# Kernel optimization log

Hardware: AMD Instinct MI355X
Metric: run time of the kernel (lower is better)

Reference implementation:

```python
import math
import jax, jax.numpy as jnp
import numpy as np

B, T, D = 32, 2048, 512
FACTOR = 2
TOP_K = int(FACTOR * math.log(T))  # = 15, static (T is static under jit)


def setup_inputs() -> dict:
    key = jax.random.key(0)
    ks = jax.random.split(key, 11)
    s = 1.0 / math.sqrt(D)
    return {
        "query": jax.random.normal(ks[0], (B, T, D), jnp.float32),
        "key_in": jax.random.normal(ks[1], (B, T, D), jnp.float32),
        "value": jax.random.normal(ks[2], (B, T, D), jnp.float32),
        "Wq": jax.random.normal(ks[3], (D, D), jnp.float32) * s,
        "bq": jnp.zeros((D,), jnp.float32),
        "Wk": jax.random.normal(ks[4], (D, D), jnp.float32) * s,
        "bk": jnp.zeros((D,), jnp.float32),
        "Wv": jax.random.normal(ks[5], (D, D), jnp.float32) * s,
        "bv": jnp.zeros((D,), jnp.float32),
        "Wo": jax.random.normal(ks[6], (D, D), jnp.float32) * s,
        "bo": jnp.zeros((D,), jnp.float32),
    }


def reference(query, key_in, value, Wq, bq, Wk, bk, Wv, bv, Wo, bo):
    # Linear projections (query/key/value lengths are equal here, so no trimming)
    q = query @ Wq + bq      # [B, T, D]
    k = key_in @ Wk + bk     # [B, T, D]
    v = value @ Wv + bv      # [B, T, D]

    # FFT cross-correlation along the time axis
    qf = jnp.fft.rfft(q, axis=1)
    kf = jnp.fft.rfft(k, axis=1)
    attn_weights = jnp.fft.irfft(qf * jnp.conj(kf), n=T, axis=1)  # [B, T, D]

    # Top-k delay selection on the feature-mean autocorrelation
    autocorr_mean = attn_weights.mean(axis=-1)           # [B, T]
    _, topk_delays = jax.lax.top_k(autocorr_mean, TOP_K)  # [B, K] int32

    # Sum of circularly-rolled values over the top-k delays.
    # tf.roll(v, s, 0): out[t] = v[(t - s) mod T]; accumulate via scan over K
    def body(acc, d):  # d: [B] delays for this k
        rolled = jax.vmap(lambda vb, db: jnp.roll(vb, db, axis=0))(v, d)
        return acc + rolled, None

    rolled_sum, _ = jax.lax.scan(body, jnp.zeros_like(v), topk_delays.T)  # [B, T, D]

    # Softmax over the feature axis (independent of k in the original loop)
    soft_attn = jax.nn.softmax(attn_weights, axis=-1)    # [B, T, D]
    attn_output = rolled_sum * soft_attn                 # [B, T, D]

    return attn_output @ Wo + bo
```

## Files before the change

kernel.cpp:

```cpp
#include <hip/hip_runtime.h>

#define NFFT 2048
#define LDK 40
#define FFT_PAD(p) ((p) + ((p) >> 5))

typedef __attribute__((ext_vector_type(8))) short bf16x8;
typedef __attribute__((ext_vector_type(4))) float f32x4;

__device__ __forceinline__ unsigned short f2bf_rne(float x) {
  unsigned u = __float_as_uint(x);
  return (unsigned short)((u + 0x7fffu + ((u >> 16) & 1u)) >> 16);
}
__device__ __forceinline__ float bf2f(unsigned short h) {
  return __uint_as_float(((unsigned)h) << 16);
}

__global__ __launch_bounds__(256) void wsplit_kernel(
    const float* __restrict__ W0, const float* __restrict__ W1,
    const float* __restrict__ W2, const float* __restrict__ W3,
    unsigned short* __restrict__ out) {
  __shared__ float tile[32][33];
  const float* W = (blockIdx.z == 0) ? W0
                   : (blockIdx.z == 1) ? W1
                   : (blockIdx.z == 2) ? W2 : W3;
  unsigned short* hi = out + (size_t)blockIdx.z * 524288;
  unsigned short* lo = hi + 262144;
  const int k0 = blockIdx.x * 32, n0 = blockIdx.y * 32;
  const int c = threadIdx.x & 31, r = threadIdx.x >> 5;
#pragma unroll
  for (int p = 0; p < 4; p++)
    tile[r + 8 * p][c] = W[(size_t)(k0 + r + 8 * p) * 512 + n0 + c];
  __syncthreads();
#pragma unroll
  for (int p = 0; p < 4; p++) {
    int nn = r + 8 * p;
    float x = tile[c][nn];
    unsigned u = __float_as_uint(x);
    unsigned short h = (unsigned short)(u >> 16);
    float hf = __uint_as_float(u & 0xffff0000u);
    unsigned short l = f2bf_rne(x - hf);
    hi[(size_t)(n0 + nn) * 512 + k0 + c] = h;
    lo[(size_t)(n0 + nn) * 512 + k0 + c] = l;
  }
}

__global__ __launch_bounds__(256) void proj_gemm_split(
    const float* __restrict__ X, const unsigned short* __restrict__ WThi,
    const unsigned short* __restrict__ WTlo, const float* __restrict__ bias,
    float* __restrict__ YT) {
  __shared__ __align__(16) unsigned short Wh[128 * LDK];
  __shared__ __align__(16) unsigned short Wl[128 * LDK];
  __shared__ __align__(16) unsigned short Xh[128 * LDK];
  __shared__ __align__(16) unsigned short Xl[128 * LDK];
  const int tid = threadIdx.x;
  const int n0 = blockIdx.x * 128;
  const int b = blockIdx.y >> 4;
  const int t0 = (blockIdx.y & 15) * 128;
  const int w = tid >> 6, l = tid & 63;
  const int wn = (w & 1) * 64;
  const int wt = (w >> 1) * 64;
  const int fr = l & 15;
  const int fk = (l >> 4) * 8;

  f32x4 acc[4][4];
#pragma unroll
  for (int i = 0; i < 4; i++)
#pragma unroll
    for (int j = 0; j < 4; j++) acc[i][j] = (f32x4)0.f;

  const int srow = tid >> 1, scol = (tid & 1) * 16;
  const float* Xg = X + ((size_t)(b * 2048 + t0 + srow)) * 512 + scol;
  const unsigned short* Whg = WThi + ((size_t)(n0 + srow)) * 512 + scol;
  const unsigned short* Wlg = WTlo + ((size_t)(n0 + srow)) * 512 + scol;
  unsigned short* XhL = &Xh[srow * LDK + scol];
  unsigned short* XlL = &Xl[srow * LDK + scol];
  unsigned short* WhL = &Wh[srow * LDK + scol];
  unsigned short* WlL = &Wl[srow * LDK + scol];

  for (int k0 = 0; k0 < 512; k0 += 32) {
    float xv[16];
    *(float4*)&xv[0] = *(const float4*)&Xg[k0];
    *(float4*)&xv[4] = *(const float4*)&Xg[k0 + 4];
    *(float4*)&xv[8] = *(const float4*)&Xg[k0 + 8];
    *(float4*)&xv[12] = *(const float4*)&Xg[k0 + 12];
    uint4 wh0 = *(const uint4*)&Whg[k0];
    uint4 wh1 = *(const uint4*)&Whg[k0 + 8];
    uint4 wl0 = *(const uint4*)&Wlg[k0];
    uint4 wl1 = *(const uint4*)&Wlg[k0 + 8];
    union { unsigned short us[16]; uint4 q[2]; } hb, lb;
#pragma unroll
    for (int i = 0; i < 16; i++) {
      unsigned u = __float_as_uint(xv[i]);
      hb.us[i] = (unsigned short)(u >> 16);
      float hf = __uint_as_float(u & 0xffff0000u);
      lb.us[i] = f2bf_rne(xv[i] - hf);
    }
    __syncthreads();
    *(uint4*)&XhL[0] = hb.q[0];
    *(uint4*)&XhL[8] = hb.q[1];
    *(uint4*)&XlL[0] = lb.q[0];
    *(uint4*)&XlL[8] = lb.q[1];
    *(uint4*)&WhL[0] = wh0;
    *(uint4*)&WhL[8] = wh1;
    *(uint4*)&WlL[0] = wl0;
    *(uint4*)&WlL[8] = wl1;
    __syncthreads();
    bf16x8 ah[4], al[4], bh[4], bl[4];
#pragma unroll
    for (int i = 0; i < 4; i++) {
      ah[i] = *(const bf16x8*)&Wh[(wn + 16 * i + fr) * LDK + fk];
      al[i] = *(const bf16x8*)&Wl[(wn + 16 * i + fr) * LDK + fk];
      bh[i] = *(const bf16x8*)&Xh[(wt + 16 * i + fr) * LDK + fk];
      bl[i] = *(const bf16x8*)&Xl[(wt + 16 * i + fr) * LDK + fk];
    }
#pragma unroll
    for (int i = 0; i < 4; i++)
#pragma unroll
      for (int j = 0; j < 4; j++) {
        acc[i][j] = __builtin_amdgcn_mfma_f32_16x16x32_bf16(ah[i], bh[j],
                                                            acc[i][j], 0, 0, 0);
        acc[i][j] = __builtin_amdgcn_mfma_f32_16x16x32_bf16(al[i], bh[j],
                                                            acc[i][j], 0, 0, 0);
        acc[i][j] = __builtin_amdgcn_mfma_f32_16x16x32_bf16(ah[i], bl[j],
                                                            acc[i][j], 0, 0, 0);
      }
  }
  const size_t obase = (size_t)b * 512 * 2048;
#pragma unroll
  for (int i = 0; i < 4; i++) {
#pragma unroll
    for (int r = 0; r < 4; r++) {
      int n = n0 + wn + 16 * i + (l >> 4) * 4 + r;
      float bsc = bias[n];
      size_t row = obase + (size_t)n * 2048 + t0 + wt + (l & 15);
#pragma unroll
      for (int j = 0; j < 4; j++) YT[row + 16 * j] = acc[i][j][r] + bsc;
    }
  }
}

__global__ __launch_bounds__(256) void gemm_bf16_vproj(
    const float* __restrict__ X, const unsigned short* __restrict__ WThi,
    const float* __restrict__ bias, unsigned short* __restrict__ Vbf) {
  __shared__ __align__(16) unsigned short Ws[128 * LDK];
  __shared__ __align__(16) unsigned short Xs[128 * LDK];
  const int tid = threadIdx.x;
  const int n0 = blockIdx.x * 128;
  const int b = blockIdx.y >> 4;
  const int t0 = (blockIdx.y & 15) * 128;
  const int w = tid >> 6, l = tid & 63;
  const int wr = (w & 1) * 64;
  const int wc = (w >> 1) * 64;
  const int fr = l & 15, fk = (l >> 4) * 8;

  f32x4 acc[4][4];
#pragma unroll
  for (int i = 0; i < 4; i++)
#pragma unroll
    for (int j = 0; j < 4; j++) acc[i][j] = (f32x4)0.f;

  const int srow = tid >> 1, scol = (tid & 1) * 16;
  const float* Xg = X + ((size_t)(b * 2048 + t0 + srow)) * 512 + scol;
  const unsigned short* Wg = WThi + ((size_t)(n0 + srow)) * 512 + scol;
  unsigned short* XsL = &Xs[srow * LDK + scol];
  unsigned short* WsL = &Ws[srow * LDK + scol];

  for (int k0 = 0; k0 < 512; k0 += 32) {
    float xv[16];
    *(float4*)&xv[0] = *(const float4*)&Xg[k0];
    *(float4*)&xv[4] = *(const float4*)&Xg[k0 + 4];
    *(float4*)&xv[8] = *(const float4*)&Xg[k0 + 8];
    *(float4*)&xv[12] = *(const float4*)&Xg[k0 + 12];
    uint4 w0 = *(const uint4*)&Wg[k0];
    uint4 w1 = *(const uint4*)&Wg[k0 + 8];
    union { unsigned short us[16]; uint4 q[2]; } hb;
#pragma unroll
    for (int i = 0; i < 16; i++) hb.us[i] = f2bf_rne(xv[i]);
    __syncthreads();
    *(uint4*)&XsL[0] = hb.q[0];
    *(uint4*)&XsL[8] = hb.q[1];
    *(uint4*)&WsL[0] = w0;
    *(uint4*)&WsL[8] = w1;
    __syncthreads();
    bf16x8 af[4], bf[4];
#pragma unroll
    for (int i = 0; i < 4; i++) {
      af[i] = *(const bf16x8*)&Xs[(wr + 16 * i + fr) * LDK + fk];
      bf[i] = *(const bf16x8*)&Ws[(wc + 16 * i + fr) * LDK + fk];
    }
#pragma unroll
    for (int i = 0; i < 4; i++)
#pragma unroll
      for (int j = 0; j < 4; j++)
        acc[i][j] = __builtin_amdgcn_mfma_f32_16x16x32_bf16(af[i], bf[j],
                                                            acc[i][j], 0, 0, 0);
  }
  float bj[4];
#pragma unroll
  for (int j = 0; j < 4; j++) bj[j] = bias[n0 + wc + 16 * j + (l & 15)];
#pragma unroll
  for (int i = 0; i < 4; i++) {
#pragma unroll
    for (int r = 0; r < 4; r++) {
      int t = t0 + wr + 16 * i + (l >> 4) * 4 + r;
      unsigned short* vrow = Vbf + ((size_t)(b * 2048 + t)) * 512;
#pragma unroll
      for (int j = 0; j < 4; j++) {
        int d = n0 + wc + 16 * j + (l & 15);
        vrow[d] = f2bf_rne(acc[i][j][r] + bj[j]);
      }
    }
  }
}

__global__ __launch_bounds__(256) void gemm_bf16_out(
    const unsigned short* __restrict__ Abf,
    const unsigned short* __restrict__ WThi, const float* __restrict__ bias,
    float* __restrict__ Y) {
  __shared__ __align__(16) unsigned short Ws[128 * LDK];
  __shared__ __align__(16) unsigned short Xs[128 * LDK];
  const int tid = threadIdx.x;
  const int n0 = blockIdx.x * 128;
  const int b = blockIdx.y >> 4;
  const int t0 = (blockIdx.y & 15) * 128;
  const int w = tid >> 6, l = tid & 63;
  const int wr = (w & 1) * 64;
  const int wc = (w >> 1) * 64;
  const int fr = l & 15, fk = (l >> 4) * 8;

  f32x4 acc[4][4];
#pragma unroll
  for (int i = 0; i < 4; i++)
#pragma unroll
    for (int j = 0; j < 4; j++) acc[i][j] = (f32x4)0.f;

  const int srow = tid >> 1, scol = (tid & 1) * 16;
  const unsigned short* Ag = Abf + ((size_t)(b * 2048 + t0 + srow)) * 512 + scol;
  const unsigned short* Wg = WThi + ((size_t)(n0 + srow)) * 512 + scol;
  unsigned short* XsL = &Xs[srow * LDK + scol];
  unsigned short* WsL = &Ws[srow * LDK + scol];

  for (int k0 = 0; k0 < 512; k0 += 32) {
    uint4 a0 = *(const uint4*)&Ag[k0];
    uint4 a1 = *(const uint4*)&Ag[k0 + 8];
    uint4 w0 = *(const uint4*)&Wg[k0];
    uint4 w1 = *(const uint4*)&Wg[k0 + 8];
    __syncthreads();
    *(uint4*)&XsL[0] = a0;
    *(uint4*)&XsL[8] = a1;
    *(uint4*)&WsL[0] = w0;
    *(uint4*)&WsL[8] = w1;
    __syncthreads();
    bf16x8 af[4], bf[4];
#pragma unroll
    for (int i = 0; i < 4; i++) {
      af[i] = *(const bf16x8*)&Xs[(wr + 16 * i + fr) * LDK + fk];
      bf[i] = *(const bf16x8*)&Ws[(wc + 16 * i + fr) * LDK + fk];
    }
#pragma unroll
    for (int i = 0; i < 4; i++)
#pragma unroll
      for (int j = 0; j < 4; j++)
        acc[i][j] = __builtin_amdgcn_mfma_f32_16x16x32_bf16(af[i], bf[j],
                                                            acc[i][j], 0, 0, 0);
  }
  float bj[4];
#pragma unroll
  for (int j = 0; j < 4; j++) bj[j] = bias[n0 + wc + 16 * j + (l & 15)];
#pragma unroll
  for (int i = 0; i < 4; i++) {
#pragma unroll
    for (int r = 0; r < 4; r++) {
      int t = t0 + wr + 16 * i + (l >> 4) * 4 + r;
      float* yrow = Y + ((size_t)(b * 2048 + t)) * 512;
#pragma unroll
      for (int j = 0; j < 4; j++) {
        int n = n0 + wc + 16 * j + (l & 15);
        yrow[n] = acc[i][j][r] + bj[j];
      }
    }
  }
}

__device__ __forceinline__ float2 cadd(float2 a, float2 b) {
  return make_float2(a.x + b.x, a.y + b.y);
}
__device__ __forceinline__ float2 csub(float2 a, float2 b) {
  return make_float2(a.x - b.x, a.y - b.y);
}
__device__ __forceinline__ float2 cmulf(float2 a, float2 b) {
  return make_float2(a.x * b.x - a.y * b.y, a.x * b.y + a.y * b.x);
}
template <int SGN>
__device__ __forceinline__ float2 mul_i(float2 a) {
  return (SGN < 0) ? make_float2(a.y, -a.x) : make_float2(-a.y, a.x);
}

template <int SGN>
__device__ __forceinline__ void dft4(float2 v[4]) {
  float2 b0 = cadd(v[0], v[2]);
  float2 b2 = csub(v[0], v[2]);
  float2 b1 = cadd(v[1], v[3]);
  float2 b3 = mul_i<SGN>(csub(v[1], v[3]));
  v[0] = cadd(b0, b1);
  v[2] = csub(b0, b1);
  v[1] = cadd(b2, b3);
  v[3] = csub(b2, b3);
}

template <int SGN>
__device__ __forceinline__ void dft8(float2 v[8]) {
  const float C = 0.70710678118654752f;
  float2 e[4], o[4];
#pragma unroll
  for (int i = 0; i < 4; i++) {
    e[i] = cadd(v[i], v[i + 4]);
    o[i] = csub(v[i], v[i + 4]);
  }
  {
    float s = o[1].x, t = o[1].y;
    o[1] = (SGN < 0) ? make_float2(C * (s + t), C * (t - s))
                     : make_float2(C * (s - t), C * (s + t));
  }
  o[2] = mul_i<SGN>(o[2]);
  {
    float s = o[3].x, t = o[3].y;
    o[3] = (SGN < 0) ? make_float2(C * (t - s), -C * (s + t))
                     : make_float2(-C * (s + t), C * (s - t));
  }
  dft4<SGN>(e);
  dft4<SGN>(o);
  v[0] = e[0]; v[2] = e[1]; v[4] = e[2]; v[6] = e[3];
  v[1] = o[0]; v[3] = o[1]; v[5] = o[2]; v[7] = o[3];
}

__device__ __forceinline__ void twiddle8_pair(float2 vz[8], float2 vw[8],
                                              float ang) {
  float2 T;
  __sincosf(ang, &T.y, &T.x);
  float2 t = T;
  vz[1] = cmulf(vz[1], t);
  vw[1] = cmulf(vw[1], t);
#pragma unroll
  for (int r = 2; r < 8; r++) {
    t = cmulf(t, T);
    vz[r] = cmulf(vz[r], t);
    vw[r] = cmulf(vw[r], t);
  }
}
__device__ __forceinline__ void twiddle8_one(float2 v[8], float ang) {
  float2 T;
  __sincosf(ang, &T.y, &T.x);
  float2 t = T;
  v[1] = cmulf(v[1], t);
#pragma unroll
  for (int r = 2; r < 8; r++) {
    t = cmulf(t, T);
    v[r] = cmulf(v[r], t);
  }
}

__global__ __launch_bounds__(256) void fft_correlate(
    float* __restrict__ qT, const float* __restrict__ kT) {
  __shared__ float2 ldsZ[2112];
  __shared__ float2 ldsW[2112];
  const int b = blockIdx.x;
  const int d0 = blockIdx.y * 2;
  const int tid = threadIdx.x;
  const size_t base = ((size_t)b * 512 + d0) * 2048;

  const float W1 = -6.28318530717958647692f / 2048.f;
  const int j2 = tid & 31, j3 = tid & 3;
  const int s1 = tid >> 5, s2 = tid >> 2;
  const int f1 = ((tid & 7) << 6) | (tid & 56) | (tid >> 6);
  const int pt = tid + (tid >> 5);
  const int b2 = 264 * s1 + j2;
  const int b3 = 33 * s2 + j3;

  float2 vz[8], vw[8];
#pragma unroll
  for (int r = 0; r < 8; r++) {
    int t = tid + (r << 8);
    vz[r] = make_float2(qT[base + t], qT[base + 2048 + t]);
    vw[r] = make_float2(kT[base + t], kT[base + 2048 + t]);
  }

  dft8<-1>(vz);
  dft8<-1>(vw);
  twiddle8_pair(vz, vw, W1 * (float)tid);
#pragma unroll
  for (int r = 0; r < 8; r++) {
    ldsZ[pt + 264 * r] = vz[r];
    ldsW[pt + 264 * r] = vw[r];
  }
  __syncthreads();
#pragma unroll
  for (int m = 0; m < 8; m++) {
    vz[m] = ldsZ[b2 + 33 * m];
    vw[m] = ldsW[b2 + 33 * m];
  }
  dft8<-1>(vz);
  dft8<-1>(vw);
  twiddle8_pair(vz, vw, (W1 * 8.f) * (float)j2);
#pragma unroll
  for (int r = 0; r < 8; r++) {
    ldsZ[b2 + 33 * r] = vz[r];
    ldsW[b2 + 33 * r] = vw[r];
  }
  __syncthreads();
#pragma unroll
  for (int m = 0; m < 8; m++) {
    vz[m] = ldsZ[b3 + 4 * m];
    vw[m] = ldsW[b3 + 4 * m];
  }
  dft8<-1>(vz);
  dft8<-1>(vw);
  twiddle8_pair(vz, vw, (W1 * 64.f) * (float)j3);
#pragma unroll
  for (int r = 0; r < 8; r++) {
    ldsZ[b3 + 4 * r] = vz[r];
    ldsW[b3 + 4 * r] = vw[r];
  }
  __syncthreads();
  {
    float2 za[4], zb[4], wa[4], wb[4];
    const int pb = f1 << 2;
#pragma unroll
    for (int c = 0; c < 4; c++) {
      za[c] = ldsZ[FFT_PAD(pb + c)];
      zb[c] = ldsZ[FFT_PAD(pb + 16 + c)];
      wa[c] = ldsW[FFT_PAD(pb + c)];
      wb[c] = ldsW[FFT_PAD(pb + 16 + c)];
    }
    dft4<-1>(za);
    dft4<-1>(zb);
    dft4<-1>(wa);
    dft4<-1>(wb);
    __syncthreads();
#pragma unroll
    for (int c = 0; c < 4; c++) {
      ldsZ[pt + 528 * c] = za[c];
      ldsZ[pt + 264 + 528 * c] = zb[c];
      ldsW[pt + 528 * c] = wa[c];
      ldsW[pt + 264 + 528 * c] = wb[c];
    }
  }
  __syncthreads();

  float2 G[8];
#pragma unroll
  for (int r = 0; r < 8; r++) {
    int f = tid + (r << 8);
    int fn = (NFFT - f) & (NFFT - 1);
    float2 Zf = ldsZ[pt + 264 * r], Zn = ldsZ[FFT_PAD(fn)];
    float2 Wf = ldsW[pt + 264 * r], Wn = ldsW[FFT_PAD(fn)];
    float A1x = Zf.x + Zn.x, A1y = Zf.y - Zn.y;
    float B1x = Wf.x + Wn.x, B1y = Wn.y - Wf.y;
    float A2x = Zf.x - Zn.x, A2y = Zf.y + Zn.y;
    float B2x = Wf.x - Wn.x, B2y = -Wf.y - Wn.y;
    float p1x = A1x * B1x - A1y * B1y;
    float p1y = A1x * B1y + A1y * B1x;
    float p2x = A2x * B2x - A2y * B2y;
    float p2y = A2x * B2y + A2y * B2x;
    G[r] = make_float2(0.25f * (p1x - p2y), 0.25f * (p1y + p2x));
    (void)f;
  }
  __syncthreads();

  dft8<1>(G);
  twiddle8_one(G, (-W1) * (float)tid);
#pragma unroll
  for (int r = 0; r < 8; r++) ldsZ[pt + 264 * r] = G[r];
  __syncthreads();
#pragma unroll
  for (int m = 0; m < 8; m++) G[m] = ldsZ[b2 + 33 * m];
  dft8<1>(G);
  twiddle8_one(G, (-W1 * 8.f) * (float)j2);
#pragma unroll
  for (int r = 0; r < 8; r++) ldsZ[b2 + 33 * r] = G[r];
  __syncthreads();
#pragma unroll
  for (int m = 0; m < 8; m++) G[m] = ldsZ[b3 + 4 * m];
  dft8<1>(G);
  twiddle8_one(G, (-W1 * 64.f) * (float)j3);
#pragma unroll
  for (int r = 0; r < 8; r++) ldsZ[b3 + 4 * r] = G[r];
  __syncthreads();
  {
    float2 za[4], zb[4];
    const int pb = f1 << 2;
#pragma unroll
    for (int c = 0; c < 4; c++) {
      za[c] = ldsZ[FFT_PAD(pb + c)];
      zb[c] = ldsZ[FFT_PAD(pb + 16 + c)];
    }
    dft4<1>(za);
    dft4<1>(zb);
    const float scale = 1.0f / (float)NFFT;
#pragma unroll
    for (int c = 0; c < 4; c++) {
      int ta = tid + (c << 9);
      int tb = ta + 256;
      qT[base + ta] = za[c].x * scale;
      qT[base + 2048 + ta] = za[c].y * scale;
      qT[base + tb] = zb[c].x * scale;
      qT[base + 2048 + tb] = zb[c].y * scale;
    }
  }
}

__global__ __launch_bounds__(256) void colstats_kernel(
    const float* __restrict__ attnT, float* __restrict__ mean,
    float2* __restrict__ stats) {
  const int b = blockIdx.x;
  const int t = blockIdx.y * 256 + threadIdx.x;
  const size_t base = (size_t)b * 512 * 2048 + t;
  float sum = 0.f, m = -1e30f, s = 0.f;
  for (int d = 0; d < 512; d++) {
    float a = attnT[base + (size_t)d * 2048];
    sum += a;
    float mn = fmaxf(m, a);
    s = s * __expf(m - mn) + __expf(a - mn);
    m = mn;
  }
  mean[b * 2048 + t] = sum * (1.f / 512.f);
  stats[b * 2048 + t] = make_float2(m, s);
}

__global__ __launch_bounds__(256) void topk_kernel(
    const float* __restrict__ mean, int* __restrict__ delays) {
  __shared__ float vals[2048];
  __shared__ float sv[256];
  __shared__ int si[256];
  const int b = blockIdx.x, tid = threadIdx.x;
#pragma unroll
  for (int r = 0; r < 8; r++)
    vals[tid + (r << 8)] = mean[b * 2048 + tid + (r << 8)];
  __syncthreads();
  for (int k = 0; k < 15; k++) {
    float bv = -1e30f;
    int bi = 1 << 30;
#pragma unroll
    for (int r = 0; r < 8; r++) {
      int i = (r << 8) + tid;
      float v = vals[i];
      if (v > bv || (v == bv && i < bi)) { bv = v; bi = i; }
    }
    sv[tid] = bv;
    si[tid] = bi;
    __syncthreads();
    for (int off = 128; off > 0; off >>= 1) {
      if (tid < off) {
        float v2 = sv[tid + off];
        int i2 = si[tid + off];
        if (v2 > sv[tid] || (v2 == sv[tid] && i2 < si[tid])) {
          sv[tid] = v2;
          si[tid] = i2;
        }
      }
      __syncthreads();
    }
    if (tid == 0) {
      delays[b * 15 + k] = si[0];
      vals[si[0]] = -1e30f;
    }
    __syncthreads();
  }
}

__global__ __launch_bounds__(256) void ctx_kernel(
    const float* __restrict__ attnT, const unsigned short* __restrict__ vbf,
    const float2* __restrict__ stats, const int* __restrict__ delays,
    unsigned short* __restrict__ ctx) {
  const int b = blockIdx.x;
  const int tb = blockIdx.y * 8;
  const int tid = threadIdx.x;
  __shared__ int dly[15];
  if (tid < 15) dly[tid] = delays[b * 15 + tid];
  __syncthreads();
  const size_t vbase = (size_t)b * 2048 * 512;
  const size_t abase = (size_t)b * 512 * 2048;
#pragma unroll
  for (int half = 0; half < 2; half++) {
    int d = half * 256 + tid;
    for (int tt = 0; tt < 8; tt++) {
      int t = tb + tt;
      float rolled = 0.f;
#pragma unroll
      for (int k = 0; k < 15; k++)
        rolled += bf2f(vbf[vbase + (size_t)((t - dly[k]) & 2047) * 512 + d]);
      float2 st = stats[b * 2048 + t];
      float a = attnT[abase + (size_t)d * 2048 + t];
      float p = __expf(a - st.x) / st.y;
      ctx[vbase + (size_t)t * 512 + d] = f2bf_rne(p * rolled);
    }
  }
}

extern "C" void kernel_launch(void* const* d_in, const int* in_sizes, int n_in,
                              void* d_out, int out_size, void* d_ws,
                              size_t ws_size, hipStream_t stream) {
  const float* query = (const float*)d_in[0];
  const float* key_in = (const float*)d_in[1];
  const float* value = (const float*)d_in[2];
  const float* Wq = (const float*)d_in[3];
  const float* bq = (const float*)d_in[4];
  const float* Wk = (const float*)d_in[5];
  const float* bk = (const float*)d_in[6];
  const float* Wv = (const float*)d_in[7];
  const float* bv = (const float*)d_in[8];
  const float* Wo = (const float*)d_in[9];
  const float* bo = (const float*)d_in[10];
  float* out = (float*)d_out;

  float* ws = (float*)d_ws;
  const size_t SZ = (size_t)32 * 512 * 2048;
  float* qT = ws;
  float* kT = ws + SZ;
  unsigned short* vbf = (unsigned short*)(ws + SZ);
  unsigned short* ctxbf = (unsigned short*)(ws + SZ + SZ / 2);
  unsigned short* wbuf = (unsigned short*)(ws + 2 * SZ);
  float* mean = ws + 2 * SZ + 1048576;
  float2* stats = (float2*)(ws + 2 * SZ + 1048576 + 65536);
  int* delays = (int*)(ws + 2 * SZ + 1048576 + 65536 + 131072);

  const unsigned short* wq_hi = wbuf + 0 * 524288;
  const unsigned short* wq_lo = wq_hi + 262144;
  const unsigned short* wk_hi = wbuf + 1 * 524288;
  const unsigned short* wk_lo = wk_hi + 262144;
  const unsigned short* wv_hi = wbuf + 2 * 524288;
  const unsigned short* wo_hi = wbuf + 3 * 524288;

  wsplit_kernel<<<dim3(16, 16, 4), 256, 0, stream>>>(Wq, Wk, Wv, Wo, wbuf);

  proj_gemm_split<<<dim3(4, 512), 256, 0, stream>>>(query, wq_hi, wq_lo, bq, qT);
  proj_gemm_split<<<dim3(4, 512), 256, 0, stream>>>(key_in, wk_hi, wk_lo, bk, kT);

  fft_correlate<<<dim3(32, 256), 256, 0, stream>>>(qT, kT);

  gemm_bf16_vproj<<<dim3(4, 512), 256, 0, stream>>>(value, wv_hi, bv, vbf);

  colstats_kernel<<<dim3(32, 8), 256, 0, stream>>>(qT, mean, stats);
  topk_kernel<<<32, 256, 0, stream>>>(mean, delays);
  ctx_kernel<<<dim3(32, 256), 256, 0, stream>>>(qT, vbf, stats, delays, ctxbf);

  gemm_bf16_out<<<dim3(4, 512), 256, 0, stream>>>(ctxbf, wo_hi, bo, out);
}
```

Measured before the change: 1.205 ms.

## Rewrite ctx kernel with LDS-transposed attention tiles and vectorized bf16 value gathers

The context kernel now processes a 64-timestep tile per block. It stages the transposed attention slice through a padded shared-memory tile so global reads become coalesced float4 loads instead of strided column accesses. Each thread reads 16 contiguous bf16 values per delay with 128-bit loads, precomputes row offsets and the softmax reciprocal, and writes outputs with vector stores. Block indices are remapped so batches are interleaved within each group, which may help L2 locality; the cost is more registers and extra barriers per feature chunk.

```diff
diff --git a/kernel.cpp b/kernel.cpp
--- a/kernel.cpp
+++ b/kernel.cpp
@@ -572,28 +572,70 @@
     const float* __restrict__ attnT, const unsigned short* __restrict__ vbf,
     const float2* __restrict__ stats, const int* __restrict__ delays,
     unsigned short* __restrict__ ctx) {
-  const int b = blockIdx.x;
-  const int tb = blockIdx.y * 8;
+  __shared__ float atile[64][65];
+  __shared__ int dly[15];
+  const int lin = blockIdx.x;
+  const int g = lin >> 8;
+  const int r = lin & 255;
+  const int b = g * 8 + (r & 7);
+  const int tb = (r >> 3) * 64;
   const int tid = threadIdx.x;
-  __shared__ int dly[15];
   if (tid < 15) dly[tid] = delays[b * 15 + tid];
   __syncthreads();
+
+  const int tl = tid >> 2;
+  const int dq = (tid & 3) * 16;
+  const int tq = (tid & 3) * 4;
+  const int t = tb + tl;
+  const float2 st = stats[b * 2048 + t];
+  const float m = st.x, inv_s = 1.f / st.y;
+
+  int rowoff[15];
+#pragma unroll
+  for (int k = 0; k < 15; k++)
+    rowoff[k] = ((t - dly[k]) & 2047) * 512;
+
   const size_t vbase = (size_t)b * 2048 * 512;
   const size_t abase = (size_t)b * 512 * 2048;
-#pragma unroll
-  for (int half = 0; half < 2; half++) {
-    int d = half * 256 + tid;
-    for (int tt = 0; tt < 8; tt++) {
-      int t = tb + tt;
-      float rolled = 0.f;
-#pragma unroll
-      for (int k = 0; k < 15; k++)
-        rolled += bf2f(vbf[vbase + (size_t)((t - dly[k]) & 2047) * 512 + d]);
-      float2 st = stats[b * 2048 + t];
-      float a = attnT[abase + (size_t)d * 2048 + t];
-      float p = __expf(a - st.x) / st.y;
-      ctx[vbase + (size_t)t * 512 + d] = f2bf_rne(p * rolled);
-    }
+
+  for (int d0 = 0; d0 < 512; d0 += 64) {
+    __syncthreads();
+#pragma unroll
+    for (int tt = 0; tt < 4; tt++) {
+      float4 a4 = *(const float4*)&attnT[abase + (size_t)(d0 + tl) * 2048 +
+                                         tb + tt * 16 + tq];
+      atile[tt * 16 + tq + 0][tl] = a4.x;
+      atile[tt * 16 + tq + 1][tl] = a4.y;
+      atile[tt * 16 + tq + 2][tl] = a4.z;
+      atile[tt * 16 + tq + 3][tl] = a4.w;
+    }
+    __syncthreads();
+
+    float rolled[16];
+#pragma unroll
+    for (int i = 0; i < 16; i++) rolled[i] = 0.f;
+#pragma unroll
+    for (int k = 0; k < 15; k++) {
+      const uint4* vp = (const uint4*)(vbf + vbase + rowoff[k] + d0 + dq);
+      uint4 v0 = vp[0], v1 = vp[1];
+      unsigned uu[8] = {v0.x, v0.y, v0.z, v0.w, v1.x, v1.y, v1.z, v1.w};
+#pragma unroll
+      for (int w = 0; w < 8; w++) {
+        rolled[2 * w + 0] += __uint_as_float(uu[w] << 16);
+        rolled[2 * w + 1] += __uint_as_float(uu[w] & 0xffff0000u);
+      }
+    }
+
+    union { unsigned short us[16]; uint4 q[2]; } ob;
+#pragma unroll
+    for (int i = 0; i < 16; i++) {
+      float a = atile[tl][dq + i];
+      float p = __expf(a - m) * inv_s;
+      ob.us[i] = f2bf_rne(p * rolled[i]);
+    }
+    uint4* op = (uint4*)(ctx + vbase + (size_t)t * 512 + d0 + dq);
+    op[0] = ob.q[0];
+    op[1] = ob.q[1];
   }
 }
 
@@ -642,7 +684,7 @@
 
   colstats_kernel<<<dim3(32, 8), 256, 0, stream>>>(qT, mean, stats);
   topk_kernel<<<32, 256, 0, stream>>>(mean, delays);
-  ctx_kernel<<<dim3(32, 256), 256, 0, stream>>>(qT, vbf, stats, delays, ctxbf);
+  ctx_kernel<<<1024, 256, 0, stream>>>(qT, vbf, stats, delays, ctxbf);
 
   gemm_bf16_out<<<dim3(4, 512), 256, 0, stream>>>(ctxbf, wo_hi, bo, out);
 }
```

Measured after the change: 1.056 ms. 1.14x faster.
